# Optimization experiments

Measured on AMD Instinct MI355X. Metric: run time of the kernel, lower is better.

Reference implementation:

```python
import jax, jax.numpy as jnp
import numpy as np

D_MODEL = 1024
H = 16
D_K = D_MODEL // H  # 64
B = 4
NQ = 1024
NK = 1024


def setup_inputs() -> dict:
    key = jax.random.key(0)
    ks = jax.random.split(key, 16)
    inp = {
        "queries": jax.random.normal(ks[0], (B, NQ, D_MODEL), jnp.float32),
        "keys": jax.random.normal(ks[1], (B, NK, D_MODEL), jnp.float32),
        "values": jax.random.normal(ks[2], (B, NK, D_MODEL), jnp.float32),
        "attention_weights": jax.random.uniform(ks[3], (B, H, NQ, NK), jnp.float32),
        "attention_mask": jax.random.randint(ks[4], (B, H, NQ, NK), 0, 2).astype(bool),
        # Linear params, init.normal_(std=0.001), zero bias (torch Linear: y = x @ W.T + b)
        "Wq": 0.001 * jax.random.normal(ks[5], (D_MODEL, D_MODEL), jnp.float32),
        "bq": jnp.zeros((D_MODEL,), jnp.float32),
        "Wk": 0.001 * jax.random.normal(ks[6], (D_MODEL, D_MODEL), jnp.float32),
        "bk": jnp.zeros((D_MODEL,), jnp.float32),
        "Wv": 0.001 * jax.random.normal(ks[7], (D_MODEL, D_MODEL), jnp.float32),
        "bv": jnp.zeros((D_MODEL,), jnp.float32),
        "Wo": 0.001 * jax.random.normal(ks[8], (D_MODEL, D_MODEL), jnp.float32),
        "bo": jnp.zeros((D_MODEL,), jnp.float32),
    }
    return inp


def reference(queries, keys, values, attention_weights, attention_mask,
              Wq, bq, Wk, bk, Wv, bv, Wo, bo):
    b_s, nq, _ = queries.shape
    nk = keys.shape[1]
    # projections -> (b, h, n, d_k)
    q = (queries @ Wq.T + bq).reshape(b_s, nq, H, D_K).transpose(0, 2, 1, 3)
    k = (keys @ Wk.T + bk).reshape(b_s, nk, H, D_K).transpose(0, 2, 1, 3)
    v = (values @ Wv.T + bv).reshape(b_s, nk, H, D_K).transpose(0, 2, 1, 3)
    scale = 1.0 / np.sqrt(D_K).astype(np.float32)
    att = jnp.einsum("bhqd,bhkd->bhqk", q, k) * scale
    att = att * attention_weights
    att = jnp.where(attention_mask, -jnp.inf, att)
    att = jax.nn.softmax(att, axis=-1)
    # dropout is identity in eval mode
    out = jnp.einsum("bhqk,bhkd->bhqd", att, v)
    out = out.transpose(0, 2, 1, 3).reshape(b_s, nq, H * D_K)
    out = out @ Wo.T + bo
    return (out, att)
```

## Files before the change

kernel.cpp:

```cpp
#include <hip/hip_runtime.h>
#include <stdint.h>

#define B_ 4
#define H_ 16
#define NQ_ 1024
#define NK_ 1024
#define DM_ 1024
#define DK_ 64

typedef __attribute__((ext_vector_type(8))) short short8;
typedef __attribute__((ext_vector_type(4))) float f32x4;
typedef unsigned short u16;
typedef unsigned int u32;

__device__ __forceinline__ u16 f2bf(float f) {
  u32 u = __builtin_bit_cast(u32, f);
  u32 r = u + 0x7fffu + ((u >> 16) & 1u);
  return (u16)(r >> 16);
}

__device__ __forceinline__ float bf2f(u16 b) {
  u32 u = ((u32)b) << 16;
  return __builtin_bit_cast(float, u);
}

__device__ __forceinline__ short8 ld_short8(const u16* p) {
  return __builtin_bit_cast(short8, *(const int4*)p);
}

__device__ __forceinline__ int4 gload16(const void* p) {
  int4 d;
  asm volatile("global_load_dwordx4 %0, %1, off" : "=v"(d) : "v"(p));
  return d;
}
__device__ __forceinline__ int2 gload8(const void* p) {
  int2 d;
  asm volatile("global_load_dwordx2 %0, %1, off" : "=v"(d) : "v"(p));
  return d;
}
#define VMW(N) do { asm volatile("s_waitcnt vmcnt(" #N ")" ::: "memory"); \
                    __builtin_amdgcn_sched_barrier(0); } while (0)
#define LGKM_BARRIER() do { \
    asm volatile("s_waitcnt lgkmcnt(0)\n\ts_barrier" ::: "memory"); \
    __builtin_amdgcn_sched_barrier(0); } while (0)

__global__ void detect_mask_kernel(const unsigned char* __restrict__ m, int* __restrict__ flag) {
  if (threadIdx.x == 0) {
    int f = 0;
    for (int i = 0; i < 256; ++i)
      if ((i & 3) != 0 && m[i] != 0) f = 1;
    *flag = f;
  }
}

__global__ __launch_bounds__(256) void gemm_kernel(
    const float* __restrict__ Aq, const float* __restrict__ Ak, const float* __restrict__ Av,
    const u16* __restrict__ Ao,
    const float* __restrict__ Wq, const float* __restrict__ Wk,
    const float* __restrict__ Wv, const float* __restrict__ Wo,
    const float* __restrict__ bq, const float* __restrict__ bk,
    const float* __restrict__ bv, const float* __restrict__ bo,
    u16* __restrict__ qbuf, u16* __restrict__ kbuf, u16* __restrict__ vTbuf,
    float* __restrict__ outbuf, int mode_base)
{
  const int z = mode_base + (int)blockIdx.z;
  const int n0 = blockIdx.x * 128;
  const int m0 = blockIdx.y * 128;
  const int tid = threadIdx.x;
  const int lane = tid & 63;
  const int wave = tid >> 6;
  const int wm = wave >> 1, wn = wave & 1;

  __shared__ u16 Al[128 * 40];
  __shared__ u16 Bl[128 * 40];

  const float* Af = (z == 0) ? Aq : (z == 1 ? Ak : Av);
  const float* W  = (z == 0) ? Wq : (z == 1 ? Wk : (z == 2 ? Wv : Wo));

  f32x4 acc[4][4];
#pragma unroll
  for (int i = 0; i < 4; ++i)
#pragma unroll
    for (int j = 0; j < 4; ++j) acc[i][j] = (f32x4){0.f, 0.f, 0.f, 0.f};

  float4 arf[4];
  int4   arb[2];
  float4 brf[4];

  auto load_tiles = [&](int ks) {
    const int kk0 = ks * 32;
    if (z < 3) {
#pragma unroll
      for (int c = 0; c < 4; ++c) {
        int chunk = c * 256 + tid;
        arf[c] = *(const float4*)(Af + (size_t)(m0 + (chunk >> 3)) * DM_ + kk0 + (chunk & 7) * 4);
      }
    } else {
#pragma unroll
      for (int c = 0; c < 2; ++c) {
        int chunk = c * 256 + tid;
        arb[c] = *(const int4*)(Ao + (size_t)(m0 + (chunk >> 2)) * DM_ + kk0 + (chunk & 3) * 8);
      }
    }
#pragma unroll
    for (int c = 0; c < 4; ++c) {
      int chunk = c * 256 + tid;
      brf[c] = *(const float4*)(W + (size_t)(n0 + (chunk >> 3)) * DM_ + kk0 + (chunk & 7) * 4);
    }
  };

  auto store_lds = [&]() {
    if (z < 3) {
#pragma unroll
      for (int c = 0; c < 4; ++c) {
        int chunk = c * 256 + tid;
        ushort4 p;
        p.x = f2bf(arf[c].x); p.y = f2bf(arf[c].y); p.z = f2bf(arf[c].z); p.w = f2bf(arf[c].w);
        *(ushort4*)(Al + (chunk >> 3) * 40 + (chunk & 7) * 4) = p;
      }
    } else {
#pragma unroll
      for (int c = 0; c < 2; ++c) {
        int chunk = c * 256 + tid;
        *(int4*)(Al + (chunk >> 2) * 40 + (chunk & 3) * 8) = arb[c];
      }
    }
#pragma unroll
    for (int c = 0; c < 4; ++c) {
      int chunk = c * 256 + tid;
      ushort4 p;
      p.x = f2bf(brf[c].x); p.y = f2bf(brf[c].y); p.z = f2bf(brf[c].z); p.w = f2bf(brf[c].w);
      *(ushort4*)(Bl + (chunk >> 3) * 40 + (chunk & 7) * 4) = p;
    }
  };

  load_tiles(0);
  for (int ks = 0; ks < 32; ++ks) {
    __syncthreads();
    store_lds();
    __syncthreads();
    if (ks < 31) load_tiles(ks + 1);
    short8 afr[4], bfr[4];
#pragma unroll
    for (int i = 0; i < 4; ++i) {
      afr[i] = ld_short8(Al + (wm * 64 + i * 16 + (lane & 15)) * 40 + (lane >> 4) * 8);
      bfr[i] = ld_short8(Bl + (wn * 64 + i * 16 + (lane & 15)) * 40 + (lane >> 4) * 8);
    }
#pragma unroll
    for (int i = 0; i < 4; ++i)
#pragma unroll
      for (int j = 0; j < 4; ++j)
        acc[i][j] = __builtin_amdgcn_mfma_f32_16x16x32_bf16(afr[i], bfr[j], acc[i][j], 0, 0, 0);
  }

  const float* bias = (z == 0) ? bq : (z == 1 ? bk : (z == 2 ? bv : bo));
#pragma unroll
  for (int i = 0; i < 4; ++i) {
    const int token0 = m0 + wm * 64 + i * 16 + (lane >> 4) * 4;
#pragma unroll
    for (int j = 0; j < 4; ++j) {
      const int feat = n0 + wn * 64 + j * 16 + (lane & 15);
      const float bvl = bias[feat];
      if (z == 3) {
#pragma unroll
        for (int r = 0; r < 4; ++r)
          outbuf[(size_t)(token0 + r) * DM_ + feat] = acc[i][j][r] + bvl;
      } else if (z == 2) {
        const int bb = token0 >> 10, t = token0 & 1023;
        const int hh = feat >> 6, d = feat & 63;
        ushort4 p;
        p.x = f2bf(acc[i][j][0] + bvl);
        p.y = f2bf(acc[i][j][1] + bvl);
        p.z = f2bf(acc[i][j][2] + bvl);
        p.w = f2bf(acc[i][j][3] + bvl);
        *(ushort4*)(vTbuf + ((size_t)(bb * H_ + hh) * DK_ + d) * NK_ + t) = p;
      } else {
        u16* dst = (z == 0) ? qbuf : kbuf;
        const int hh = feat >> 6, d = feat & 63;
#pragma unroll
        for (int r = 0; r < 4; ++r) {
          const int token = token0 + r;
          const int bb = token >> 10, t = token & 1023;
          dst[((size_t)(bb * H_ + hh) * NQ_ + t) * DK_ + d] = f2bf(acc[i][j][r] + bvl);
        }
      }
    }
  }
}

__global__ __launch_bounds__(512) void attn_kernel(
    const u16* __restrict__ qbuf, const u16* __restrict__ kbuf, const u16* __restrict__ vTbuf,
    const float* __restrict__ aw, const void* __restrict__ maskp, const int* __restrict__ flagp,
    float* __restrict__ attout, u16* __restrict__ obuf)
{
  __shared__ u16 S[16 * 1024];

  const int n = blockIdx.x;
  const int work = (n & 7) * 512 + (n >> 3);
  const int qt = work & 63;
  const int bh = work >> 6;
  const int b = bh >> 4, h = bh & 15;
  const int qbase = qt * 16;
  const int tid = threadIdx.x;
  const int lane = tid & 63;
  const int wave = tid >> 6;
  const int hi = lane >> 4;
  const int l15 = lane & 15;
  const int mflag = *flagp;

  const int c0 = lane * 8;
  const size_t ab0 = ((size_t)bh * NQ_ + qbase + wave) * (size_t)NK_;
  const size_t ab1 = ab0 + 8 * (size_t)NK_;

  const u16* qp = qbuf + ((size_t)bh * NQ_ + qbase + l15) * DK_ + hi * 8;
  int4 qd0 = gload16(qp);
  int4 qd1 = gload16(qp + 32);

  const u16* kbase = kbuf + (size_t)bh * NK_ * DK_;
  const int tkc = wave * 16 + l15;
  int4 kq0[8], kq1[8];
#pragma unroll
  for (int t = 0; t < 8; ++t) {
    const u16* kp_ = kbase + (size_t)(t * 128 + tkc) * DK_ + hi * 8;
    kq0[t] = gload16(kp_);
    kq1[t] = gload16(kp_ + 32);
  }
  int4 a00 = gload16(aw + ab0 + c0);
  int4 a01 = gload16(aw + ab0 + c0 + 4);
  int4 a02 = gload16(aw + ab0 + c0 + 512);
  int4 a03 = gload16(aw + ab0 + c0 + 516);

  VMW(20);
  const short8 qf0 = __builtin_bit_cast(short8, qd0);
  const short8 qf1 = __builtin_bit_cast(short8, qd1);

#define QK_EAT(t) do { \
    f32x4 sacc_ = (f32x4){0.f, 0.f, 0.f, 0.f}; \
    sacc_ = __builtin_amdgcn_mfma_f32_16x16x32_bf16(qf0, __builtin_bit_cast(short8, kq0[t]), sacc_, 0, 0, 0); \
    sacc_ = __builtin_amdgcn_mfma_f32_16x16x32_bf16(qf1, __builtin_bit_cast(short8, kq1[t]), sacc_, 0, 0, 0); \
    const int tk_ = (t) * 128 + tkc; \
    _Pragma("unroll") \
    for (int r = 0; r < 4; ++r) { \
      const int row_ = hi * 4 + r; \
      S[row_ * 1024 + (tk_ ^ ((row_ & 7) << 3))] = f2bf(sacc_[r]); \
    } } while (0)

  VMW(16);  QK_EAT(0); QK_EAT(1);
  VMW(12);  QK_EAT(2); QK_EAT(3);
  VMW(8);   QK_EAT(4); QK_EAT(5);
  VMW(4);   QK_EAT(6); QK_EAT(7);
#undef QK_EAT

  LGKM_BARRIER();

  {
    const float scale = 0.125f;

#define SM_CONSUME(row_, bm_, A0_, A1_, A2_, A3_, ab_) do { \
    u16* Srow_ = S + (row_) * 1024; \
    const int swz_ = ((row_) & 7) << 3; \
    const short8 sL_ = ld_short8(Srow_ + (c0 ^ swz_)); \
    const short8 sH_ = ld_short8(Srow_ + ((c0 + 512) ^ swz_)); \
    const f32x4 awA_ = __builtin_bit_cast(f32x4, A0_); \
    const f32x4 awB_ = __builtin_bit_cast(f32x4, A1_); \
    const f32x4 awC_ = __builtin_bit_cast(f32x4, A2_); \
    const f32x4 awD_ = __builtin_bit_cast(f32x4, A3_); \
    f32x4 eA_, eB_, eC_, eD_; \
    _Pragma("unroll") \
    for (int jj = 0; jj < 4; ++jj) { \
      eA_[jj] = (((bm_) >> jj) & 1u) ? 0.f : __expf(bf2f((u16)sL_[jj]) * scale * awA_[jj]); \
      eB_[jj] = (((bm_) >> (4 + jj)) & 1u) ? 0.f : __expf(bf2f((u16)sL_[4 + jj]) * scale * awB_[jj]); \
      eC_[jj] = (((bm_) >> (8 + jj)) & 1u) ? 0.f : __expf(bf2f((u16)sH_[jj]) * scale * awC_[jj]); \
      eD_[jj] = (((bm_) >> (12 + jj)) & 1u) ? 0.f : __expf(bf2f((u16)sH_[4 + jj]) * scale * awD_[jj]); \
    } \
    float sum_ = 0.f; \
    _Pragma("unroll") \
    for (int jj = 0; jj < 4; ++jj) sum_ += (eA_[jj] + eB_[jj]) + (eC_[jj] + eD_[jj]); \
    _Pragma("unroll") \
    for (int o_ = 32; o_ >= 1; o_ >>= 1) sum_ += __shfl_xor(sum_, o_); \
    const float inv_ = 1.0f / sum_; \
    eA_ *= inv_; eB_ *= inv_; eC_ *= inv_; eD_ *= inv_; \
    *(f32x4*)(attout + (ab_) + c0) = eA_; \
    *(f32x4*)(attout + (ab_) + c0 + 4) = eB_; \
    *(f32x4*)(attout + (ab_) + c0 + 512) = eC_; \
    *(f32x4*)(attout + (ab_) + c0 + 516) = eD_; \
    short8 pL_, pH_; \
    _Pragma("unroll") \
    for (int jj = 0; jj < 4; ++jj) { \
      pL_[jj] = (short)f2bf(eA_[jj]); pL_[4 + jj] = (short)f2bf(eB_[jj]); \
      pH_[jj] = (short)f2bf(eC_[jj]); pH_[4 + jj] = (short)f2bf(eD_[jj]); \
    } \
    *(int4*)(Srow_ + (c0 ^ swz_)) = __builtin_bit_cast(int4, pL_); \
    *(int4*)(Srow_ + ((c0 + 512) ^ swz_)) = __builtin_bit_cast(int4, pH_); \
  } while (0)

    if (mflag) {
      const unsigned char* mp = (const unsigned char*)maskp;
      int2 s0a = gload8(mp + ab0 + c0);
      int2 s0b = gload8(mp + ab0 + c0 + 512);
      int2 d0a = gload8(mp + ab0 + c0);
      int2 d0b = gload8(mp + ab0 + c0 + 512);
      int4 a10 = gload16(aw + ab1 + c0);
      int4 a11 = gload16(aw + ab1 + c0 + 4);
      int4 a12 = gload16(aw + ab1 + c0 + 512);
      int4 a13 = gload16(aw + ab1 + c0 + 516);
      int2 s1a = gload8(mp + ab1 + c0);
      int2 s1b = gload8(mp + ab1 + c0 + 512);
      int2 d1a = gload8(mp + ab1 + c0);
      int2 d1b = gload8(mp + ab1 + c0 + 512);
      (void)d0a; (void)d0b; (void)d1a; (void)d1b;
      VMW(8);
      u32 bm0 = 0;
#pragma unroll
      for (int j = 0; j < 4; ++j) {
        bm0 |= (((u32)s0a.x >> (8 * j)) & 1u) << j;
        bm0 |= (((u32)s0a.y >> (8 * j)) & 1u) << (4 + j);
        bm0 |= (((u32)s0b.x >> (8 * j)) & 1u) << (8 + j);
        bm0 |= (((u32)s0b.y >> (8 * j)) & 1u) << (12 + j);
      }
      SM_CONSUME(wave, bm0, a00, a01, a02, a03, ab0);
      VMW(4);
      u32 bm1 = 0;
#pragma unroll
      for (int j = 0; j < 4; ++j) {
        bm1 |= (((u32)s1a.x >> (8 * j)) & 1u) << j;
        bm1 |= (((u32)s1a.y >> (8 * j)) & 1u) << (4 + j);
        bm1 |= (((u32)s1b.x >> (8 * j)) & 1u) << (8 + j);
        bm1 |= (((u32)s1b.y >> (8 * j)) & 1u) << (12 + j);
      }
      SM_CONSUME(wave + 8, bm1, a10, a11, a12, a13, ab1);
    } else {
      const int* mp = (const int*)maskp;
      int4 m00 = gload16(mp + ab0 + c0);
      int4 m01 = gload16(mp + ab0 + c0 + 4);
      int4 m02 = gload16(mp + ab0 + c0 + 512);
      int4 m03 = gload16(mp + ab0 + c0 + 516);
      int4 a10 = gload16(aw + ab1 + c0);
      int4 a11 = gload16(aw + ab1 + c0 + 4);
      int4 a12 = gload16(aw + ab1 + c0 + 512);
      int4 a13 = gload16(aw + ab1 + c0 + 516);
      int4 m10 = gload16(mp + ab1 + c0);
      int4 m11 = gload16(mp + ab1 + c0 + 4);
      int4 m12 = gload16(mp + ab1 + c0 + 512);
      int4 m13 = gload16(mp + ab1 + c0 + 516);
      VMW(8);
      u32 bm0 = ((u32)m00.x) | ((u32)m00.y << 1) | ((u32)m00.z << 2) | ((u32)m00.w << 3)
              | ((u32)m01.x << 4) | ((u32)m01.y << 5) | ((u32)m01.z << 6) | ((u32)m01.w << 7)
              | ((u32)m02.x << 8) | ((u32)m02.y << 9) | ((u32)m02.z << 10) | ((u32)m02.w << 11)
              | ((u32)m03.x << 12) | ((u32)m03.y << 13) | ((u32)m03.z << 14) | ((u32)m03.w << 15);
      SM_CONSUME(wave, bm0, a00, a01, a02, a03, ab0);
      VMW(4);
      u32 bm1 = ((u32)m10.x) | ((u32)m10.y << 1) | ((u32)m10.z << 2) | ((u32)m10.w << 3)
              | ((u32)m11.x << 4) | ((u32)m11.y << 5) | ((u32)m11.z << 6) | ((u32)m11.w << 7)
              | ((u32)m12.x << 8) | ((u32)m12.y << 9) | ((u32)m12.z << 10) | ((u32)m12.w << 11)
              | ((u32)m13.x << 12) | ((u32)m13.y << 13) | ((u32)m13.z << 14) | ((u32)m13.w << 15);
      SM_CONSUME(wave + 8, bm1, a10, a11, a12, a13, ab1);
    }
#undef SM_CONSUME
  }

  LGKM_BARRIER();
  VMW(0);

  {
    const int kh = wave >> 2;
    const int j = wave & 3;
    const u16* Sr = S + l15 * 1024;
    const int asw = (l15 & 7) << 3;
    const int dcol = j * 16 + l15;
    const u16* vb = vTbuf + ((size_t)bh * DK_ + dcol) * (size_t)NK_;
    const int kh512 = kh * 512;
    f32x4 o0 = (f32x4){0.f, 0.f, 0.f, 0.f};
    f32x4 o1 = (f32x4){0.f, 0.f, 0.f, 0.f};
    int4 vq[16];

#define PV_ISSUE(t) do { vq[t] = gload16(vb + kh512 + (t) * 32 + hi * 8); } while (0)
#define PV_EAT(t) do { \
    const int c_ = kh512 + (t) * 32 + hi * 8; \
    const short8 pa_ = ld_short8(Sr + (c_ ^ asw)); \
    if ((t) & 1) o1 = __builtin_amdgcn_mfma_f32_16x16x32_bf16(pa_, __builtin_bit_cast(short8, vq[t]), o1, 0, 0, 0); \
    else        o0 = __builtin_amdgcn_mfma_f32_16x16x32_bf16(pa_, __builtin_bit_cast(short8, vq[t]), o0, 0, 0, 0); \
  } while (0)

    PV_ISSUE(0); PV_ISSUE(1); PV_ISSUE(2); PV_ISSUE(3);
    PV_ISSUE(4); PV_ISSUE(5); PV_ISSUE(6); PV_ISSUE(7);
    VMW(4);
    PV_EAT(0); PV_EAT(1); PV_EAT(2); PV_EAT(3);
    PV_ISSUE(8); PV_ISSUE(9); PV_ISSUE(10); PV_ISSUE(11);
    VMW(4);
    PV_EAT(4); PV_EAT(5); PV_EAT(6); PV_EAT(7);
    PV_ISSUE(12); PV_ISSUE(13); PV_ISSUE(14); PV_ISSUE(15);
    VMW(4);
    PV_EAT(8); PV_EAT(9); PV_EAT(10); PV_EAT(11);
    VMW(0);
    PV_EAT(12); PV_EAT(13); PV_EAT(14); PV_EAT(15);
#undef PV_ISSUE
#undef PV_EAT

    f32x4 oacc = o0 + o1;
    __syncthreads();
    float* Pbuf = (float*)S;
    if (kh == 1) {
#pragma unroll
      for (int r = 0; r < 4; ++r)
        Pbuf[(hi * 4 + r) * 64 + dcol] = oacc[r];
    }
    __syncthreads();
    if (kh == 0) {
      const int feat = h * DK_ + dcol;
#pragma unroll
      for (int r = 0; r < 4; ++r) {
        const int row = hi * 4 + r;
        obuf[((size_t)b * NQ_ + qbase + row) * DM_ + feat] =
            f2bf(oacc[r] + Pbuf[row * 64 + dcol]);
      }
    }
  }
}

extern "C" void kernel_launch(void* const* d_in, const int* in_sizes, int n_in,
                              void* d_out, int out_size, void* d_ws, size_t ws_size,
                              hipStream_t stream)
{
  const float* queries = (const float*)d_in[0];
  const float* keys    = (const float*)d_in[1];
  const float* values  = (const float*)d_in[2];
  const float* aw      = (const float*)d_in[3];
  const void*  maskp   = d_in[4];
  const float* Wq = (const float*)d_in[5];
  const float* bq = (const float*)d_in[6];
  const float* Wk = (const float*)d_in[7];
  const float* bk = (const float*)d_in[8];
  const float* Wv = (const float*)d_in[9];
  const float* bv = (const float*)d_in[10];
  const float* Wo = (const float*)d_in[11];
  const float* bo = (const float*)d_in[12];

  char* ws = (char*)d_ws;
  const size_t NE = (size_t)B_ * H_ * NQ_ * DK_;
  int* flag  = (int*)ws;
  u16* qbuf  = (u16*)(ws + 256);
  u16* kbuf  = qbuf + NE;
  u16* vTbuf = kbuf + NE;
  u16* obuf  = vTbuf + NE;
  if (ws_size < 256 + 8 * NE) return;

  float* outp = (float*)d_out;
  float* attp = outp + (size_t)B_ * NQ_ * DM_;

  detect_mask_kernel<<<1, 64, 0, stream>>>((const unsigned char*)maskp, flag);

  gemm_kernel<<<dim3(8, 32, 3), 256, 0, stream>>>(queries, keys, values, obuf,
      Wq, Wk, Wv, Wo, bq, bk, bv, bo, qbuf, kbuf, vTbuf, outp, 0);

  attn_kernel<<<dim3(4096), 512, 0, stream>>>(qbuf, kbuf, vTbuf, aw, maskp, flag,
                                              attp, obuf);

  gemm_kernel<<<dim3(8, 32, 1), 256, 0, stream>>>(queries, keys, values, obuf,
      Wq, Wk, Wv, Wo, bq, bk, bv, bo, qbuf, kbuf, vTbuf, outp, 3);
}
```

Before: 349.5 us.

## Pre-convert activations to bf16 and stream GEMM A tiles via global_load_lds

A separate kernel converts queries, keys and values to bf16 in scratch space borrowed from the attention output buffer. The projection GEMM then loads A tiles straight into LDS with global_load_lds, using a 64-wide K tile and an XOR-swizzled layout in place of padded rows. Weights are still converted in registers. Register double-buffering is dropped, so global loads are no longer overlapped with MFMA, and the extra conversion pass adds traffic.

```diff
diff --git a/kernel.cpp b/kernel.cpp
--- a/kernel.cpp
+++ b/kernel.cpp
@@ -44,6 +44,12 @@
     asm volatile("s_waitcnt lgkmcnt(0)\n\ts_barrier" ::: "memory"); \
     __builtin_amdgcn_sched_barrier(0); } while (0)
 
+typedef const __attribute__((address_space(1))) unsigned int* as1_t;
+typedef __attribute__((address_space(3))) unsigned int* as3_t;
+__device__ __forceinline__ void gload_lds16(const u16* g, u16* l) {
+  __builtin_amdgcn_global_load_lds((as1_t)(const void*)g, (as3_t)(void*)l, 16, 0, 0);
+}
+
 __global__ void detect_mask_kernel(const unsigned char* __restrict__ m, int* __restrict__ flag) {
   if (threadIdx.x == 0) {
     int f = 0;
@@ -53,8 +59,29 @@
   }
 }
 
+__global__ __launch_bounds__(256) void convert_kernel(
+    const float* __restrict__ q, const float* __restrict__ k, const float* __restrict__ v,
+    u16* __restrict__ dst)
+{
+  const int y = blockIdx.y;
+  const float* src = (y == 0) ? q : (y == 1 ? k : v);
+  u16* d = dst + (size_t)y * 4194304;
+  const size_t nchunk = 4194304 / 8;
+  const size_t stride = (size_t)gridDim.x * 256;
+  for (size_t i = (size_t)blockIdx.x * 256 + threadIdx.x; i < nchunk; i += stride) {
+    const float4 f0 = *(const float4*)(src + i * 8);
+    const float4 f1 = *(const float4*)(src + i * 8 + 4);
+    short8 p;
+    p[0] = (short)f2bf(f0.x); p[1] = (short)f2bf(f0.y);
+    p[2] = (short)f2bf(f0.z); p[3] = (short)f2bf(f0.w);
+    p[4] = (short)f2bf(f1.x); p[5] = (short)f2bf(f1.y);
+    p[6] = (short)f2bf(f1.z); p[7] = (short)f2bf(f1.w);
+    *(int4*)(d + i * 8) = __builtin_bit_cast(int4, p);
+  }
+}
+
 __global__ __launch_bounds__(256) void gemm_kernel(
-    const float* __restrict__ Aq, const float* __restrict__ Ak, const float* __restrict__ Av,
+    const u16* __restrict__ Aq, const u16* __restrict__ Ak, const u16* __restrict__ Av,
     const u16* __restrict__ Ao,
     const float* __restrict__ Wq, const float* __restrict__ Wk,
     const float* __restrict__ Wv, const float* __restrict__ Wo,
@@ -70,12 +97,14 @@
   const int lane = tid & 63;
   const int wave = tid >> 6;
   const int wm = wave >> 1, wn = wave & 1;
-
-  __shared__ u16 Al[128 * 40];
-  __shared__ u16 Bl[128 * 40];
-
-  const float* Af = (z == 0) ? Aq : (z == 1 ? Ak : Av);
-  const float* W  = (z == 0) ? Wq : (z == 1 ? Wk : (z == 2 ? Wv : Wo));
+  const int l15 = lane & 15;
+  const int hi = lane >> 4;
+
+  __shared__ __attribute__((aligned(16))) u16 Al[128 * 64];
+  __shared__ __attribute__((aligned(16))) u16 Bl[128 * 64];
+
+  const u16* A = (z == 0) ? Aq : (z == 1 ? Ak : (z == 2 ? Av : Ao));
+  const float* W = (z == 0) ? Wq : (z == 1 ? Wk : (z == 2 ? Wv : Wo));
 
   f32x4 acc[4][4];
 #pragma unroll
@@ -83,83 +112,59 @@
 #pragma unroll
     for (int j = 0; j < 4; ++j) acc[i][j] = (f32x4){0.f, 0.f, 0.f, 0.f};
 
-  float4 arf[4];
-  int4   arb[2];
-  float4 brf[4];
-
-  auto load_tiles = [&](int ks) {
-    const int kk0 = ks * 32;
-    if (z < 3) {
-#pragma unroll
-      for (int c = 0; c < 4; ++c) {
-        int chunk = c * 256 + tid;
-        arf[c] = *(const float4*)(Af + (size_t)(m0 + (chunk >> 3)) * DM_ + kk0 + (chunk & 7) * 4);
+  for (int ks = 0; ks < 16; ++ks) {
+    __syncthreads();
+#pragma unroll
+    for (int c = 0; c < 4; ++c) {
+      const int p = c * 256 + tid;
+      const int row = p >> 3;
+      const int kbyte = ((p & 7) << 4) ^ ((row & 7) << 4);
+      const u16* src = A + (size_t)(m0 + row) * DM_ + ks * 64 + (kbyte >> 1);
+      gload_lds16(src, Al + p * 8);
+    }
+#pragma unroll
+    for (int c = 0; c < 4; ++c) {
+      const int p = c * 256 + tid;
+      const int row = p >> 3;
+      const float* wsrc = W + (size_t)(n0 + row) * DM_ + ks * 64 + (p & 7) * 8;
+      const float4 f0 = *(const float4*)(wsrc);
+      const float4 f1 = *(const float4*)(wsrc + 4);
+      short8 pk;
+      pk[0] = (short)f2bf(f0.x); pk[1] = (short)f2bf(f0.y);
+      pk[2] = (short)f2bf(f0.z); pk[3] = (short)f2bf(f0.w);
+      pk[4] = (short)f2bf(f1.x); pk[5] = (short)f2bf(f1.y);
+      pk[6] = (short)f2bf(f1.z); pk[7] = (short)f2bf(f1.w);
+      const int cb = (((p & 7) << 4)) ^ ((row & 7) << 4);
+      *(int4*)((char*)Bl + row * 128 + cb) = __builtin_bit_cast(int4, pk);
+    }
+    __syncthreads();
+#pragma unroll
+    for (int kk = 0; kk < 2; ++kk) {
+      short8 afr[4], bfr[4];
+#pragma unroll
+      for (int i = 0; i < 4; ++i) {
+        const int ar = wm * 64 + i * 16 + l15;
+        const int ab = (kk * 64 + hi * 16) ^ ((ar & 7) << 4);
+        afr[i] = ld_short8(Al + ar * 64 + (ab >> 1));
+        const int br = wn * 64 + i * 16 + l15;
+        const int bb = (kk * 64 + hi * 16) ^ ((br & 7) << 4);
+        bfr[i] = ld_short8(Bl + br * 64 + (bb >> 1));
       }
-    } else {
-#pragma unroll
-      for (int c = 0; c < 2; ++c) {
-        int chunk = c * 256 + tid;
-        arb[c] = *(const int4*)(Ao + (size_t)(m0 + (chunk >> 2)) * DM_ + kk0 + (chunk & 3) * 8);
-      }
-    }
-#pragma unroll
-    for (int c = 0; c < 4; ++c) {
-      int chunk = c * 256 + tid;
-      brf[c] = *(const float4*)(W + (size_t)(n0 + (chunk >> 3)) * DM_ + kk0 + (chunk & 7) * 4);
-    }
-  };
-
-  auto store_lds = [&]() {
-    if (z < 3) {
-#pragma unroll
-      for (int c = 0; c < 4; ++c) {
-        int chunk = c * 256 + tid;
-        ushort4 p;
-        p.x = f2bf(arf[c].x); p.y = f2bf(arf[c].y); p.z = f2bf(arf[c].z); p.w = f2bf(arf[c].w);
-        *(ushort4*)(Al + (chunk >> 3) * 40 + (chunk & 7) * 4) = p;
-      }
-    } else {
-#pragma unroll
-      for (int c = 0; c < 2; ++c) {
-        int chunk = c * 256 + tid;
-        *(int4*)(Al + (chunk >> 2) * 40 + (chunk & 3) * 8) = arb[c];
-      }
-    }
-#pragma unroll
-    for (int c = 0; c < 4; ++c) {
-      int chunk = c * 256 + tid;
-      ushort4 p;
-      p.x = f2bf(brf[c].x); p.y = f2bf(brf[c].y); p.z = f2bf(brf[c].z); p.w = f2bf(brf[c].w);
-      *(ushort4*)(Bl + (chunk >> 3) * 40 + (chunk & 7) * 4) = p;
-    }
-  };
-
-  load_tiles(0);
-  for (int ks = 0; ks < 32; ++ks) {
-    __syncthreads();
-    store_lds();
-    __syncthreads();
-    if (ks < 31) load_tiles(ks + 1);
-    short8 afr[4], bfr[4];
-#pragma unroll
-    for (int i = 0; i < 4; ++i) {
-      afr[i] = ld_short8(Al + (wm * 64 + i * 16 + (lane & 15)) * 40 + (lane >> 4) * 8);
-      bfr[i] = ld_short8(Bl + (wn * 64 + i * 16 + (lane & 15)) * 40 + (lane >> 4) * 8);
-    }
-#pragma unroll
-    for (int i = 0; i < 4; ++i)
-#pragma unroll
-      for (int j = 0; j < 4; ++j)
-        acc[i][j] = __builtin_amdgcn_mfma_f32_16x16x32_bf16(afr[i], bfr[j], acc[i][j], 0, 0, 0);
+#pragma unroll
+      for (int i = 0; i < 4; ++i)
+#pragma unroll
+        for (int j = 0; j < 4; ++j)
+          acc[i][j] = __builtin_amdgcn_mfma_f32_16x16x32_bf16(afr[i], bfr[j], acc[i][j], 0, 0, 0);
+    }
   }
 
   const float* bias = (z == 0) ? bq : (z == 1 ? bk : (z == 2 ? bv : bo));
 #pragma unroll
   for (int i = 0; i < 4; ++i) {
-    const int token0 = m0 + wm * 64 + i * 16 + (lane >> 4) * 4;
+    const int token0 = m0 + wm * 64 + i * 16 + hi * 4;
 #pragma unroll
     for (int j = 0; j < 4; ++j) {
-      const int feat = n0 + wn * 64 + j * 16 + (lane & 15);
+      const int feat = n0 + wn * 64 + j * 16 + l15;
       const float bvl = bias[feat];
       if (z == 3) {
 #pragma unroll
@@ -448,14 +453,21 @@
   float* outp = (float*)d_out;
   float* attp = outp + (size_t)B_ * NQ_ * DM_;
 
+  u16* cvt = (u16*)attp;
+  const u16* cq = cvt;
+  const u16* ck = cvt + NE;
+  const u16* cv = cvt + 2 * NE;
+
   detect_mask_kernel<<<1, 64, 0, stream>>>((const unsigned char*)maskp, flag);
 
-  gemm_kernel<<<dim3(8, 32, 3), 256, 0, stream>>>(queries, keys, values, obuf,
+  convert_kernel<<<dim3(512, 3), 256, 0, stream>>>(queries, keys, values, cvt);
+
+  gemm_kernel<<<dim3(8, 32, 3), 256, 0, stream>>>(cq, ck, cv, obuf,
       Wq, Wk, Wv, Wo, bq, bk, bv, bo, qbuf, kbuf, vTbuf, outp, 0);
 
   attn_kernel<<<dim3(4096), 512, 0, stream>>>(qbuf, kbuf, vTbuf, aw, maskp, flag,
                                               attp, obuf);
 
-  gemm_kernel<<<dim3(8, 32, 1), 256, 0, stream>>>(queries, keys, values, obuf,
+  gemm_kernel<<<dim3(8, 32, 1), 256, 0, stream>>>(cq, ck, cv, obuf,
       Wq, Wk, Wv, Wo, bq, bk, bv, bo, qbuf, kbuf, vTbuf, outp, 3);
 }
```

Result: no change. 356.4 us (+2.0%).

## Tile V^T in 32-key blocks and switch softmax to 4-wide contiguous lane access

Applied to the files above, without the earlier changes.

V is now stored as contiguous [kt][d][32] tiles, so each PV MFMA operand load reads from one compact 4KB block per key chunk instead of rows strided by NK. The softmax stage switches from 8 consecutive elements per lane to 4 per lane at 256-element strides, so a wave's global accesses to attention weights, mask and output are fully contiguous. In the byte-mask path the redundant duplicate mask loads are dropped and single-dword loads are used. The trade-off is narrower LDS reads and writes (8-byte instead of 16-byte) against the swizzled S buffer, plus more load instructions.

```diff
diff --git a/kernel.cpp b/kernel.cpp
--- a/kernel.cpp
+++ b/kernel.cpp
@@ -33,9 +33,9 @@
   asm volatile("global_load_dwordx4 %0, %1, off" : "=v"(d) : "v"(p));
   return d;
 }
-__device__ __forceinline__ int2 gload8(const void* p) {
-  int2 d;
-  asm volatile("global_load_dwordx2 %0, %1, off" : "=v"(d) : "v"(p));
+__device__ __forceinline__ int gload4(const void* p) {
+  int d;
+  asm volatile("global_load_dword %0, %1, off" : "=v"(d) : "v"(p));
   return d;
 }
 #define VMW(N) do { asm volatile("s_waitcnt vmcnt(" #N ")" ::: "memory"); \
@@ -168,12 +168,13 @@
       } else if (z == 2) {
         const int bb = token0 >> 10, t = token0 & 1023;
         const int hh = feat >> 6, d = feat & 63;
+        const int kt = t >> 5, kk = t & 31;
         ushort4 p;
         p.x = f2bf(acc[i][j][0] + bvl);
         p.y = f2bf(acc[i][j][1] + bvl);
         p.z = f2bf(acc[i][j][2] + bvl);
         p.w = f2bf(acc[i][j][3] + bvl);
-        *(ushort4*)(vTbuf + ((size_t)(bb * H_ + hh) * DK_ + d) * NK_ + t) = p;
+        *(ushort4*)(vTbuf + (((size_t)(bb * H_ + hh) * 32 + kt) * 64 + d) * 32 + kk) = p;
       } else {
         u16* dst = (z == 0) ? qbuf : kbuf;
         const int hh = feat >> 6, d = feat & 63;
@@ -206,9 +207,9 @@
   const int wave = tid >> 6;
   const int hi = lane >> 4;
   const int l15 = lane & 15;
+  const int l4 = lane * 4;
   const int mflag = *flagp;
 
-  const int c0 = lane * 8;
   const size_t ab0 = ((size_t)bh * NQ_ + qbase + wave) * (size_t)NK_;
   const size_t ab1 = ab0 + 8 * (size_t)NK_;
 
@@ -225,10 +226,9 @@
     kq0[t] = gload16(kp_);
     kq1[t] = gload16(kp_ + 32);
   }
-  int4 a00 = gload16(aw + ab0 + c0);
-  int4 a01 = gload16(aw + ab0 + c0 + 4);
-  int4 a02 = gload16(aw + ab0 + c0 + 512);
-  int4 a03 = gload16(aw + ab0 + c0 + 516);
+  int4 aw0[4];
+#pragma unroll
+  for (int j = 0; j < 4; ++j) aw0[j] = gload16(aw + ab0 + l4 + j * 256);
 
   VMW(20);
   const short8 qf0 = __builtin_bit_cast(short8, qd0);
@@ -256,107 +256,78 @@
   {
     const float scale = 0.125f;
 
-#define SM_CONSUME(row_, bm_, A0_, A1_, A2_, A3_, ab_) do { \
+#define SM_BODY(row_, AWV_, KV_, ab_) do { \
     u16* Srow_ = S + (row_) * 1024; \
     const int swz_ = ((row_) & 7) << 3; \
-    const short8 sL_ = ld_short8(Srow_ + (c0 ^ swz_)); \
-    const short8 sH_ = ld_short8(Srow_ + ((c0 + 512) ^ swz_)); \
-    const f32x4 awA_ = __builtin_bit_cast(f32x4, A0_); \
-    const f32x4 awB_ = __builtin_bit_cast(f32x4, A1_); \
-    const f32x4 awC_ = __builtin_bit_cast(f32x4, A2_); \
-    const f32x4 awD_ = __builtin_bit_cast(f32x4, A3_); \
-    f32x4 eA_, eB_, eC_, eD_; \
+    f32x4 e_[4]; float sum_ = 0.f; \
     _Pragma("unroll") \
-    for (int jj = 0; jj < 4; ++jj) { \
-      eA_[jj] = (((bm_) >> jj) & 1u) ? 0.f : __expf(bf2f((u16)sL_[jj]) * scale * awA_[jj]); \
-      eB_[jj] = (((bm_) >> (4 + jj)) & 1u) ? 0.f : __expf(bf2f((u16)sL_[4 + jj]) * scale * awB_[jj]); \
-      eC_[jj] = (((bm_) >> (8 + jj)) & 1u) ? 0.f : __expf(bf2f((u16)sH_[jj]) * scale * awC_[jj]); \
-      eD_[jj] = (((bm_) >> (12 + jj)) & 1u) ? 0.f : __expf(bf2f((u16)sH_[4 + jj]) * scale * awD_[jj]); \
+    for (int j = 0; j < 4; ++j) { \
+      const int c_ = l4 + j * 256; \
+      const ushort4 s4_ = *(const ushort4*)(Srow_ + (c_ ^ swz_)); \
+      const f32x4 a4_ = __builtin_bit_cast(f32x4, AWV_[j]); \
+      f32x4 t_; \
+      t_[0] = KV_[j].x ? 0.f : __expf(bf2f(s4_.x) * scale * a4_[0]); \
+      t_[1] = KV_[j].y ? 0.f : __expf(bf2f(s4_.y) * scale * a4_[1]); \
+      t_[2] = KV_[j].z ? 0.f : __expf(bf2f(s4_.z) * scale * a4_[2]); \
+      t_[3] = KV_[j].w ? 0.f : __expf(bf2f(s4_.w) * scale * a4_[3]); \
+      e_[j] = t_; \
+      sum_ += (t_[0] + t_[1]) + (t_[2] + t_[3]); \
     } \
-    float sum_ = 0.f; \
-    _Pragma("unroll") \
-    for (int jj = 0; jj < 4; ++jj) sum_ += (eA_[jj] + eB_[jj]) + (eC_[jj] + eD_[jj]); \
     _Pragma("unroll") \
     for (int o_ = 32; o_ >= 1; o_ >>= 1) sum_ += __shfl_xor(sum_, o_); \
     const float inv_ = 1.0f / sum_; \
-    eA_ *= inv_; eB_ *= inv_; eC_ *= inv_; eD_ *= inv_; \
-    *(f32x4*)(attout + (ab_) + c0) = eA_; \
-    *(f32x4*)(attout + (ab_) + c0 + 4) = eB_; \
-    *(f32x4*)(attout + (ab_) + c0 + 512) = eC_; \
-    *(f32x4*)(attout + (ab_) + c0 + 516) = eD_; \
-    short8 pL_, pH_; \
     _Pragma("unroll") \
-    for (int jj = 0; jj < 4; ++jj) { \
-      pL_[jj] = (short)f2bf(eA_[jj]); pL_[4 + jj] = (short)f2bf(eB_[jj]); \
-      pH_[jj] = (short)f2bf(eC_[jj]); pH_[4 + jj] = (short)f2bf(eD_[jj]); \
+    for (int j = 0; j < 4; ++j) { \
+      const int c_ = l4 + j * 256; \
+      f32x4 t_ = e_[j]; \
+      t_[0] *= inv_; t_[1] *= inv_; t_[2] *= inv_; t_[3] *= inv_; \
+      *(f32x4*)(attout + (ab_) + c_) = t_; \
+      ushort4 p_; \
+      p_.x = f2bf(t_[0]); p_.y = f2bf(t_[1]); p_.z = f2bf(t_[2]); p_.w = f2bf(t_[3]); \
+      *(ushort4*)(Srow_ + (c_ ^ swz_)) = p_; \
     } \
-    *(int4*)(Srow_ + (c0 ^ swz_)) = __builtin_bit_cast(int4, pL_); \
-    *(int4*)(Srow_ + ((c0 + 512) ^ swz_)) = __builtin_bit_cast(int4, pH_); \
   } while (0)
 
     if (mflag) {
       const unsigned char* mp = (const unsigned char*)maskp;
-      int2 s0a = gload8(mp + ab0 + c0);
-      int2 s0b = gload8(mp + ab0 + c0 + 512);
-      int2 d0a = gload8(mp + ab0 + c0);
-      int2 d0b = gload8(mp + ab0 + c0 + 512);
-      int4 a10 = gload16(aw + ab1 + c0);
-      int4 a11 = gload16(aw + ab1 + c0 + 4);
-      int4 a12 = gload16(aw + ab1 + c0 + 512);
-      int4 a13 = gload16(aw + ab1 + c0 + 516);
-      int2 s1a = gload8(mp + ab1 + c0);
-      int2 s1b = gload8(mp + ab1 + c0 + 512);
-      int2 d1a = gload8(mp + ab1 + c0);
-      int2 d1b = gload8(mp + ab1 + c0 + 512);
-      (void)d0a; (void)d0b; (void)d1a; (void)d1b;
+      int mb0[4], mb1[4];
+      int4 aw1[4];
+#pragma unroll
+      for (int j = 0; j < 4; ++j) mb0[j] = gload4(mp + ab0 + l4 + j * 256);
+#pragma unroll
+      for (int j = 0; j < 4; ++j) aw1[j] = gload16(aw + ab1 + l4 + j * 256);
+#pragma unroll
+      for (int j = 0; j < 4; ++j) mb1[j] = gload4(mp + ab1 + l4 + j * 256);
       VMW(8);
-      u32 bm0 = 0;
+      int4 k0[4], k1[4];
 #pragma unroll
       for (int j = 0; j < 4; ++j) {
-        bm0 |= (((u32)s0a.x >> (8 * j)) & 1u) << j;
-        bm0 |= (((u32)s0a.y >> (8 * j)) & 1u) << (4 + j);
-        bm0 |= (((u32)s0b.x >> (8 * j)) & 1u) << (8 + j);
-        bm0 |= (((u32)s0b.y >> (8 * j)) & 1u) << (12 + j);
-      }
-      SM_CONSUME(wave, bm0, a00, a01, a02, a03, ab0);
+        k0[j].x = mb0[j] & 0xff;          k0[j].y = (mb0[j] >> 8) & 0xff;
+        k0[j].z = (mb0[j] >> 16) & 0xff;  k0[j].w = (mb0[j] >> 24) & 0xff;
+      }
+      SM_BODY(wave, aw0, k0, ab0);
       VMW(4);
-      u32 bm1 = 0;
 #pragma unroll
       for (int j = 0; j < 4; ++j) {
-        bm1 |= (((u32)s1a.x >> (8 * j)) & 1u) << j;
-        bm1 |= (((u32)s1a.y >> (8 * j)) & 1u) << (4 + j);
-        bm1 |= (((u32)s1b.x >> (8 * j)) & 1u) << (8 + j);
-        bm1 |= (((u32)s1b.y >> (8 * j)) & 1u) << (12 + j);
-      }
-      SM_CONSUME(wave + 8, bm1, a10, a11, a12, a13, ab1);
+        k1[j].x = mb1[j] & 0xff;          k1[j].y = (mb1[j] >> 8) & 0xff;
+        k1[j].z = (mb1[j] >> 16) & 0xff;  k1[j].w = (mb1[j] >> 24) & 0xff;
+      }
+      SM_BODY(wave + 8, aw1, k1, ab1);
     } else {
       const int* mp = (const int*)maskp;
-      int4 m00 = gload16(mp + ab0 + c0);
-      int4 m01 = gload16(mp + ab0 + c0 + 4);
-      int4 m02 = gload16(mp + ab0 + c0 + 512);
-      int4 m03 = gload16(mp + ab0 + c0 + 516);
-      int4 a10 = gload16(aw + ab1 + c0);
-      int4 a11 = gload16(aw + ab1 + c0 + 4);
-      int4 a12 = gload16(aw + ab1 + c0 + 512);
-      int4 a13 = gload16(aw + ab1 + c0 + 516);
-      int4 m10 = gload16(mp + ab1 + c0);
-      int4 m11 = gload16(mp + ab1 + c0 + 4);
-      int4 m12 = gload16(mp + ab1 + c0 + 512);
-      int4 m13 = gload16(mp + ab1 + c0 + 516);
+      int4 k0[4], aw1[4], k1[4];
+#pragma unroll
+      for (int j = 0; j < 4; ++j) k0[j] = gload16(mp + ab0 + l4 + j * 256);
+#pragma unroll
+      for (int j = 0; j < 4; ++j) aw1[j] = gload16(aw + ab1 + l4 + j * 256);
+#pragma unroll
+      for (int j = 0; j < 4; ++j) k1[j] = gload16(mp + ab1 + l4 + j * 256);
       VMW(8);
-      u32 bm0 = ((u32)m00.x) | ((u32)m00.y << 1) | ((u32)m00.z << 2) | ((u32)m00.w << 3)
-              | ((u32)m01.x << 4) | ((u32)m01.y << 5) | ((u32)m01.z << 6) | ((u32)m01.w << 7)
-              | ((u32)m02.x << 8) | ((u32)m02.y << 9) | ((u32)m02.z << 10) | ((u32)m02.w << 11)
-              | ((u32)m03.x << 12) | ((u32)m03.y << 13) | ((u32)m03.z << 14) | ((u32)m03.w << 15);
-      SM_CONSUME(wave, bm0, a00, a01, a02, a03, ab0);
+      SM_BODY(wave, aw0, k0, ab0);
       VMW(4);
-      u32 bm1 = ((u32)m10.x) | ((u32)m10.y << 1) | ((u32)m10.z << 2) | ((u32)m10.w << 3)
-              | ((u32)m11.x << 4) | ((u32)m11.y << 5) | ((u32)m11.z << 6) | ((u32)m11.w << 7)
-              | ((u32)m12.x << 8) | ((u32)m12.y << 9) | ((u32)m12.z << 10) | ((u32)m12.w << 11)
-              | ((u32)m13.x << 12) | ((u32)m13.y << 13) | ((u32)m13.z << 14) | ((u32)m13.w << 15);
-      SM_CONSUME(wave + 8, bm1, a10, a11, a12, a13, ab1);
-    }
-#undef SM_CONSUME
+      SM_BODY(wave + 8, aw1, k1, ab1);
+    }
+#undef SM_BODY
   }
 
   LGKM_BARRIER();
@@ -368,13 +339,14 @@
     const u16* Sr = S + l15 * 1024;
     const int asw = (l15 & 7) << 3;
     const int dcol = j * 16 + l15;
-    const u16* vb = vTbuf + ((size_t)bh * DK_ + dcol) * (size_t)NK_;
+    const u16* vb2 = vTbuf + (size_t)bh * (NK_ * DK_);
     const int kh512 = kh * 512;
     f32x4 o0 = (f32x4){0.f, 0.f, 0.f, 0.f};
     f32x4 o1 = (f32x4){0.f, 0.f, 0.f, 0.f};
     int4 vq[16];
 
-#define PV_ISSUE(t) do { vq[t] = gload16(vb + kh512 + (t) * 32 + hi * 8); } while (0)
+#define PV_ISSUE(t) do { \
+    vq[t] = gload16(vb2 + ((size_t)(kh * 16 + (t)) * 64 + dcol) * 32 + hi * 8); } while (0)
 #define PV_EAT(t) do { \
     const int c_ = kh512 + (t) * 32 + hi * 8; \
     const short8 pa_ = ld_short8(Sr + (c_ ^ asw)); \
```

After: 321.1 us. 8.1% less time.
